# Performance work log

Hardware: AMD Instinct MI355X
Metric: run time of the kernel (lower is better)

Reference implementation:

```python
import jax, jax.numpy as jnp
import numpy as np

T, B = 50, 512
S, A, BEL, H, E, M = 256, 32, 1024, 1024, 1024, 256
MIN_STD = 0.1


def setup_inputs() -> dict:
    key = jax.random.key(0)
    ks = jax.random.split(key, 24)
    def rn(k, shape, scale=1.0):
        return jax.random.normal(k, shape, dtype=jnp.float32) * scale
    w = 0.05  # weight init scale
    return {
        "prev_state": rn(ks[0], (B, S)),
        "actions": rn(ks[1], (T, B, A)),
        "prev_belief": rn(ks[2], (B, BEL)),
        "observations": rn(ks[3], (T, B, E)),
        "nonterminals": jnp.ones((T, B, 1), dtype=jnp.float32),
        "map_embeddings": rn(ks[4], (T, B, M)),
        "map_embeddings_post": rn(ks[5], (T, B, M)),
        "noise_prior": rn(ks[6], (T, B, S)),
        "noise_post": rn(ks[7], (T, B, S)),
        "W_sa": rn(ks[8], (BEL, S + A + M), w), "b_sa": jnp.zeros((BEL,), jnp.float32),
        "W_ih": rn(ks[9], (3 * BEL, BEL), w), "b_ih": jnp.zeros((3 * BEL,), jnp.float32),
        "W_hh": rn(ks[10], (3 * BEL, BEL), w), "b_hh": jnp.zeros((3 * BEL,), jnp.float32),
        "W_bp": rn(ks[11], (H, BEL), w), "b_bp": jnp.zeros((H,), jnp.float32),
        "W_sp": rn(ks[12], (2 * S, H), w), "b_sp": jnp.zeros((2 * S,), jnp.float32),
        "W_bq": rn(ks[13], (H, BEL + E + M), w), "b_bq": jnp.zeros((H,), jnp.float32),
        "W_sq": rn(ks[14], (2 * S, H), w), "b_sq": jnp.zeros((2 * S,), jnp.float32),
    }


def reference(prev_state, actions, prev_belief, observations, nonterminals,
              map_embeddings, map_embeddings_post, noise_prior, noise_post,
              W_sa, b_sa, W_ih, b_ih, W_hh, b_hh,
              W_bp, b_bp, W_sp, b_sp, W_bq, b_bq, W_sq, b_sq):
    relu = jax.nn.relu
    def lin(x, W, b):
        return x @ W.T + b

    def gru(x, h):  # torch.nn.GRUCell math
        gi = x @ W_ih.T + b_ih
        gh = h @ W_hh.T + b_hh
        i_r, i_z, i_n = jnp.split(gi, 3, axis=1)
        h_r, h_z, h_n = jnp.split(gh, 3, axis=1)
        r = jax.nn.sigmoid(i_r + h_r)
        z = jax.nn.sigmoid(i_z + h_z)
        n = jnp.tanh(i_n + r * h_n)
        return (1.0 - z) * n + z * h

    def std(raw):
        return jnp.minimum(jax.nn.softplus(raw) + MIN_STD, 5.0)

    def step(carry, xs):
        belief, post_state = carry
        a, obs, nt, me, mp, np_, nq = xs
        s = post_state * nt
        hid = relu(lin(jnp.concatenate([s, a, me], axis=1), W_sa, b_sa))
        belief = gru(hid, belief)
        # prior p(z_t | h_t)
        hp = relu(lin(belief, W_bp, b_bp))
        p_mean, p_raw = jnp.split(lin(hp, W_sp, b_sp), 2, axis=1)
        p_std = std(p_raw)
        p_state = p_mean + p_std * np_
        # posterior q(z_t | h_t, e_t, m_t)
        hq = relu(lin(jnp.concatenate([belief, obs, mp], axis=1), W_bq, b_bq))
        q_mean, q_raw = jnp.split(lin(hq, W_sq, b_sq), 2, axis=1)
        q_std = std(q_raw)
        q_state = q_mean + q_std * nq
        return (belief, q_state), (belief, p_state, p_mean, p_std, q_state, q_mean, q_std)

    _, outs = jax.lax.scan(
        step, (prev_belief, prev_state),
        (actions, observations, nonterminals, map_embeddings,
         map_embeddings_post, noise_prior, noise_post))
    return outs  # 7 arrays, each (T, B, *)
```

## Files before the change

### kernel.cpp

```cpp
#include <hip/hip_runtime.h>
#include <hip/hip_bf16.h>

#define NT 50
#define NB 512
#define SD 256
#define BD 1024
#define HD 1024
#define ED 1024
#define MD 256
#define NBLK 512
#define PGSZ (1024 * 256)
#define K1BIG 0x40000000

typedef __attribute__((ext_vector_type(8))) short bf16x8;
typedef __attribute__((ext_vector_type(4))) float f32x4;

__device__ __forceinline__ void gload_lds16(const void* g, void* l) {
  __builtin_amdgcn_global_load_lds(
      (const __attribute__((address_space(1))) void*)g,
      (__attribute__((address_space(3))) void*)l, 16, 0, 0);
}
__device__ __forceinline__ void gload_lds16_sc0(const void* g, void* l) {
  __builtin_amdgcn_global_load_lds(
      (const __attribute__((address_space(1))) void*)g,
      (__attribute__((address_space(3))) void*)l, 16, 0, 1);
}

__device__ __forceinline__ void aload16(const void* a, f32x4* r) {
  asm volatile("global_load_dwordx4 %0, %1, off sc0" : "=&v"(*r) : "v"(a) : "memory");
}
__device__ __forceinline__ void aload4(const void* a, float* r) {
  asm volatile("global_load_dword %0, %1, off sc0" : "=&v"(*r) : "v"(a) : "memory");
}
#define VMWAIT(N)                                        \
  asm volatile("s_waitcnt vmcnt(" #N ")" ::: "memory");  \
  __builtin_amdgcn_sched_barrier(0);

__device__ __forceinline__ void astore16(void* g, f32x4 v) {
  asm volatile("global_store_dwordx4 %0, %1, off sc0" :: "v"(g), "v"(v) : "memory");
}
__device__ __forceinline__ void astore4(void* g, float v) {
  asm volatile("global_store_dword %0, %1, off sc0" :: "v"(g), "v"(v) : "memory");
}
__device__ __forceinline__ void astore2(void* g, unsigned v) {
  asm volatile("global_store_short %0, %1, off sc0" :: "v"(g), "v"(v) : "memory");
}
__device__ __forceinline__ void ntstore16(void* g, f32x4 v) {
  asm volatile("global_store_dwordx4 %0, %1, off nt" :: "v"(g), "v"(v) : "memory");
}
__device__ __forceinline__ void ntstore4(void* g, float v) {
  asm volatile("global_store_dword %0, %1, off nt" :: "v"(g), "v"(v) : "memory");
}

__device__ __forceinline__ float sigmoidf_(float x) { return 1.0f / (1.0f + __expf(-x)); }
__device__ __forceinline__ float softplusf_(float x) {
  return (x > 0.0f) ? (x + log1pf(__expf(-x))) : log1pf(__expf(x));
}
__device__ __forceinline__ unsigned short bfb(float x) {
  __hip_bfloat16 h = __float2bfloat16(x);
  return __builtin_bit_cast(unsigned short, h);
}

__device__ __forceinline__ void xbar(unsigned* cnt, int inst, int xcd, int nx) {
  asm volatile("s_waitcnt vmcnt(0) lgkmcnt(0)" ::: "memory");
  __syncthreads();
  if (threadIdx.x == 0) {
    unsigned* c = cnt + 256 + (size_t)(inst * 8 + xcd) * 16;
    __hip_atomic_fetch_add(c, 1u, __ATOMIC_RELAXED, __HIP_MEMORY_SCOPE_AGENT);
    while (__hip_atomic_load(c, __ATOMIC_RELAXED, __HIP_MEMORY_SCOPE_AGENT) < (unsigned)nx)
      __builtin_amdgcn_s_sleep(2);
  }
  __syncthreads();
}

__device__ __noinline__ void gemm64(
    int EPI, char* lds,
    const __hip_bfloat16* __restrict__ A1, int lda1,
    const __hip_bfloat16* __restrict__ A2, int lda2, int K1,
    const __hip_bfloat16* __restrict__ Wr, int ldw, int nIter,
    const float* __restrict__ bias, const float* __restrict__ Cadd,
    float* __restrict__ Cf, __hip_bfloat16* __restrict__ Cb, int ldc, int m0) {
  const int tid = threadIdx.x;
  const int lane = tid & 63, w = tid >> 6;
  const int wr = w >> 1, wc = w & 1;
  f32x4 acc[2][2] = {};
  const __hip_bfloat16* a1r = A1 + (size_t)(m0 + lane) * lda1;
  const __hip_bfloat16* a2r = A2 ? (A2 + (size_t)(m0 + lane) * lda2) : a1r;
  const __hip_bfloat16* wrow = Wr + (size_t)lane * ldw;

  auto stage = [&](int it) {
    const int k0 = it << 6;
    char* la = lds + (size_t)(it % 3) * 16384;
    char* lb = la + 8192;
    const __hip_bfloat16* as = (k0 < K1) ? (a1r + k0) : (a2r + (k0 - K1));
    gload_lds16_sc0(as + (2 * w) * 8, la + (2 * w) * 1024);
    gload_lds16_sc0(as + (2 * w + 1) * 8, la + (2 * w + 1) * 1024);
    gload_lds16(wrow + k0 + (2 * w) * 8, lb + (2 * w) * 1024);
    gload_lds16(wrow + k0 + (2 * w + 1) * 8, lb + (2 * w + 1) * 1024);
  };

  __syncthreads();
  stage(0);
  stage(1);
  VMWAIT(4)
  __builtin_amdgcn_s_barrier();
  __builtin_amdgcn_sched_barrier(0);

  const int kq = lane >> 4, r15 = lane & 15;
  for (int i = 0; i < nIter; ++i) {
    if (i + 2 < nIter) stage(i + 2);
    const char* la = lds + (size_t)(i % 3) * 16384;
    const char* lb = la + 8192;
#pragma unroll
    for (int s = 0; s < 2; ++s) {
      bf16x8 af[2], bfr[2];
#pragma unroll
      for (int m = 0; m < 2; ++m)
        af[m] = *(const bf16x8*)(la + (size_t)((s * 4 + kq) * 64 + wr * 32 + m * 16 + r15) * 16);
#pragma unroll
      for (int n = 0; n < 2; ++n)
        bfr[n] = *(const bf16x8*)(lb + (size_t)((s * 4 + kq) * 64 + wc * 32 + n * 16 + r15) * 16);
#pragma unroll
      for (int m = 0; m < 2; ++m)
#pragma unroll
        for (int n = 0; n < 2; ++n)
          acc[m][n] = __builtin_amdgcn_mfma_f32_16x16x32_bf16(af[m], bfr[n], acc[m][n], 0, 0, 0);
    }
    if (i + 1 < nIter) {
      if (i + 2 < nIter) {
        VMWAIT(4)
      } else {
        VMWAIT(0)
      }
      __builtin_amdgcn_s_barrier();
      __builtin_amdgcn_sched_barrier(0);
    }
  }

  const int rg = lane >> 4;
  float ad[2][2][4];
  if (EPI == 3) {
#pragma unroll
    for (int m = 0; m < 2; ++m)
#pragma unroll
      for (int n = 0; n < 2; ++n) {
        const int col = wc * 32 + n * 16 + r15;
#pragma unroll
        for (int i2 = 0; i2 < 4; ++i2) {
          const int row = m0 + wr * 32 + m * 16 + rg * 4 + i2;
          aload4(Cadd + (size_t)row * ldc + col, &ad[m][n][i2]);
        }
      }
    VMWAIT(0)
  }
#pragma unroll
  for (int m = 0; m < 2; ++m) {
#pragma unroll
    for (int n = 0; n < 2; ++n) {
      const int col = wc * 32 + n * 16 + r15;
      const float bv = bias ? bias[col] : 0.0f;
#pragma unroll
      for (int i2 = 0; i2 < 4; ++i2) {
        const int row = m0 + wr * 32 + m * 16 + rg * 4 + i2;
        float v = acc[m][n][i2] + bv;
        if (EPI == 3) v += ad[m][n][i2];
        if (EPI != 0) {
          v = v > 0.0f ? v : 0.0f;
          astore2(Cb + (size_t)row * ldc + col, (unsigned)bfb(v));
        } else {
          astore4(Cf + (size_t)row * ldc + col, v);
        }
      }
    }
  }
}

__device__ __noinline__ void gemm_head64(
    char* lds, const __hip_bfloat16* __restrict__ A,
    const __hip_bfloat16* __restrict__ Wr, const float* __restrict__ bias,
    const float* __restrict__ noise, float* __restrict__ st_o, float* __restrict__ mn_o,
    float* __restrict__ sd_o, const float* __restrict__ ntn,
    __hip_bfloat16* __restrict__ sprev, int isq, int n0, int m0) {
  const int tid = threadIdx.x;
  const int lane = tid & 63, w = tid >> 6;
  const int wr = w >> 1, wc = w & 1;
  f32x4 acc[2][2] = {};
  const __hip_bfloat16* ar = A + (size_t)(m0 + lane) * BD;
  const __hip_bfloat16* wrow = Wr + (size_t)lane * BD;

  auto stage = [&](int it) {
    const int k0 = it << 6;
    char* la = lds + (size_t)(it % 3) * 16384;
    char* lb = la + 8192;
    gload_lds16_sc0(ar + k0 + (2 * w) * 8, la + (2 * w) * 1024);
    gload_lds16_sc0(ar + k0 + (2 * w + 1) * 8, la + (2 * w + 1) * 1024);
    gload_lds16(wrow + k0 + (2 * w) * 8, lb + (2 * w) * 1024);
    gload_lds16(wrow + k0 + (2 * w + 1) * 8, lb + (2 * w + 1) * 1024);
  };

  __syncthreads();
  stage(0);
  stage(1);
  VMWAIT(4)
  __builtin_amdgcn_s_barrier();
  __builtin_amdgcn_sched_barrier(0);

  const int kq = lane >> 4, r15 = lane & 15;
  for (int i = 0; i < 16; ++i) {
    if (i + 2 < 16) stage(i + 2);
    const char* la = lds + (size_t)(i % 3) * 16384;
    const char* lb = la + 8192;
#pragma unroll
    for (int s = 0; s < 2; ++s) {
      bf16x8 af[2], bfr[2];
#pragma unroll
      for (int m = 0; m < 2; ++m)
        af[m] = *(const bf16x8*)(la + (size_t)((s * 4 + kq) * 64 + wr * 32 + m * 16 + r15) * 16);
#pragma unroll
      for (int n = 0; n < 2; ++n)
        bfr[n] = *(const bf16x8*)(lb + (size_t)((s * 4 + kq) * 64 + wc * 32 + n * 16 + r15) * 16);
#pragma unroll
      for (int m = 0; m < 2; ++m)
#pragma unroll
        for (int n = 0; n < 2; ++n)
          acc[m][n] = __builtin_amdgcn_mfma_f32_16x16x32_bf16(af[m], bfr[n], acc[m][n], 0, 0, 0);
    }
    if (i + 1 < 16) {
      if (i + 2 < 16) {
        VMWAIT(4)
      } else {
        VMWAIT(0)
      }
      __builtin_amdgcn_s_barrier();
      __builtin_amdgcn_sched_barrier(0);
    }
  }

  const int rg = lane >> 4;
  const bool even = (r15 & 1) == 0;
#pragma unroll
  for (int m = 0; m < 2; ++m) {
#pragma unroll
    for (int n = 0; n < 2; ++n) {
      const int col = n0 + wc * 32 + n * 16 + r15;
      const int j = col >> 1;
      const float bv = bias[col];
#pragma unroll
      for (int i2 = 0; i2 < 4; ++i2) {
        const int row = m0 + wr * 32 + m * 16 + rg * 4 + i2;
        float v = acc[m][n][i2] + bv;
        float partner = __shfl_xor(v, 1);
        float mean = even ? v : partner;
        float raw = even ? partner : v;
        float sd = fminf(softplusf_(raw) + 0.1f, 5.0f);
        const size_t o = (size_t)row * SD + j;
        if (even) {
          float st = mean + sd * noise[o];
          ntstore4(mn_o + o, mean);
          ntstore4(st_o + o, st);
          if (isq) astore2(sprev + o, (unsigned)bfb(st * ntn[row]));
        } else {
          ntstore4(sd_o + o, sd);
        }
      }
    }
  }
}

struct Args {
  const float *prev_state, *actions, *prev_belief, *observations, *nonterminals,
      *me, *mp, *noise_p, *noise_q,
      *W_sa, *b_sa, *W_ih, *b_ih, *W_hh, *b_hh,
      *W_bp, *b_bp, *W_sp, *b_sp, *W_bq, *b_bq, *W_sq, *b_sq;
  float* out;
  unsigned* cnt;
  __hip_bfloat16 *Wsa, *Wih, *Whh, *Wbp, *Wbq, *Wsp, *Wsq;
  __hip_bfloat16 *actme, *obsmp, *sprev, *bel, *hid, *hpb, *hqb;
  float *gi, *gh, *hq_obs;
  float *bsp_ro, *bsq_ro;
};

__global__ __launch_bounds__(256) void prep(Args P) {
  const int gtid = blockIdx.x * 256 + threadIdx.x;
  for (int i = gtid; i < BD * 576; i += PGSZ) {
    int r = i / 576, k = i - r * 576;
    P.Wsa[i] = __float2bfloat16(k < 544 ? P.W_sa[(size_t)r * 544 + k] : 0.0f);
  }
  for (int i = gtid; i < 3 * BD * BD; i += PGSZ) P.Wih[i] = __float2bfloat16(P.W_ih[i]);
  for (int i = gtid; i < 3 * BD * BD; i += PGSZ) P.Whh[i] = __float2bfloat16(P.W_hh[i]);
  for (int i = gtid; i < HD * BD; i += PGSZ) P.Wbp[i] = __float2bfloat16(P.W_bp[i]);
  for (int i = gtid; i < HD * 2304; i += PGSZ) P.Wbq[i] = __float2bfloat16(P.W_bq[i]);
  for (int i = gtid; i < 512 * HD; i += PGSZ) {
    int r = i >> 10, k = i & 1023;
    int dr = (r < 256) ? (2 * r) : (2 * (r - 256) + 1);
    P.Wsp[(size_t)dr * 1024 + k] = __float2bfloat16(P.W_sp[i]);
    P.Wsq[(size_t)dr * 1024 + k] = __float2bfloat16(P.W_sq[i]);
  }
  for (int i = gtid; i < 512; i += PGSZ) {
    int dr = (i < 256) ? (2 * i) : (2 * (i - 256) + 1);
    P.bsp_ro[dr] = P.b_sp[i];
    P.bsq_ro[dr] = P.b_sq[i];
  }
  for (int i = gtid; i < NT * NB * 320; i += PGSZ) {
    int tb = i / 320, j = i - tb * 320;
    float v = (j < 32) ? P.actions[(size_t)tb * 32 + j]
                       : (j < 288 ? P.me[(size_t)tb * 256 + (j - 32)] : 0.0f);
    P.actme[i] = __float2bfloat16(v);
  }
  for (int i = gtid; i < NB * 1280; i += PGSZ) {
    int bb = i / 1280, j = i - bb * 1280;
    float v = (j < ED) ? P.observations[(size_t)bb * ED + j] : P.mp[(size_t)bb * MD + (j - ED)];
    P.obsmp[i] = __float2bfloat16(v);
  }
  for (int i = gtid; i < NB * SD; i += PGSZ) {
    int r = i >> 8;
    P.sprev[i] = __float2bfloat16(P.prev_state[i] * P.nonterminals[r]);
  }
  for (int i = gtid; i < NB * BD; i += PGSZ) P.bel[i] = __float2bfloat16(P.prev_belief[i]);
}

__global__ __launch_bounds__(256, 2) void mega(Args P) {
  __shared__ alignas(16) char lds[49152];
  __shared__ int sh[3];
  const int tid = threadIdx.x;

  if (tid == 0) {
    unsigned x;
    asm volatile("s_getreg_b32 %0, hwreg(HW_REG_XCC_ID)" : "=s"(x));
    x &= 7u;
    unsigned s = __hip_atomic_fetch_add(P.cnt + x * 16, 1u, __ATOMIC_RELAXED,
                                        __HIP_MEMORY_SCOPE_AGENT);
    sh[0] = (int)x;
    sh[1] = (int)s;
  }
  __syncthreads();
  const int xcd = sh[0], slot = sh[1];

  if (tid == 0) {
    __hip_atomic_fetch_add(P.cnt + 128, 1u, __ATOMIC_RELAXED, __HIP_MEMORY_SCOPE_AGENT);
    while (__hip_atomic_load(P.cnt + 128, __ATOMIC_RELAXED, __HIP_MEMORY_SCOPE_AGENT) <
           (unsigned)NBLK)
      __builtin_amdgcn_s_sleep(4);
    sh[2] = (int)__hip_atomic_load(P.cnt + xcd * 16, __ATOMIC_RELAXED,
                                   __HIP_MEMORY_SCOPE_AGENT);
  }
  __syncthreads();
  const int nx = sh[2];
  const int m0 = xcd * 64;
  const size_t o_ps = (size_t)NT * NB * BD;
  const size_t blk = (size_t)NT * NB * SD;

  for (int t = 0; t < NT; ++t) {
    const int inst = t * 5;
    for (int tt = slot; tt < 64; tt += nx) {
      if (tt < 16) {
        const int n = tt;
        gemm64(1, lds, P.sprev, SD, P.actme + (size_t)t * NB * 320, 320, 256,
               P.Wsa + (size_t)n * 64 * 576, 576, 9,
               P.b_sa + n * 64, nullptr, nullptr, P.hid + n * 64, BD, m0);
      } else {
        const int n = tt - 16;
        gemm64(0, lds, P.bel, BD, nullptr, 0, K1BIG,
               P.Whh + (size_t)n * 64 * BD, BD, 16,
               P.b_hh + n * 64, nullptr, P.gh + n * 64, nullptr, 3 * BD, m0);
      }
    }
    xbar(P.cnt, inst + 0, xcd, nx);
    for (int tt = slot; tt < 64; tt += nx) {
      if (tt < 48) {
        const int n = tt;
        gemm64(0, lds, P.hid, BD, nullptr, 0, K1BIG,
               P.Wih + (size_t)n * 64 * BD, BD, 16,
               P.b_ih + n * 64, nullptr, P.gi + n * 64, nullptr, 3 * BD, m0);
      } else {
        const int n = tt - 48;
        gemm64(0, lds, P.obsmp, 1280, nullptr, 0, K1BIG,
               P.Wbq + (size_t)n * 64 * 2304 + 1024, 2304, 20,
               nullptr, nullptr, P.hq_obs + n * 64, nullptr, 1024, m0);
      }
    }
    xbar(P.cnt, inst + 1, xcd, nx);
    for (int u = slot * 256 + tid; u < 8192; u += nx * 256) {
      const int r = m0 + (u >> 7), j0 = (u & 127) << 3;
      const float* gib = P.gi + (size_t)r * 3072 + j0;
      const float* ghb = P.gh + (size_t)r * 3072 + j0;
      f32x4 ir0, ir1, iz0, iz1, in0, in1, hr0, hr1, hz0, hz1, hn0, hn1, hbv;
      aload16(gib, &ir0);
      aload16(gib + 4, &ir1);
      aload16(gib + 1024, &iz0);
      aload16(gib + 1028, &iz1);
      aload16(gib + 2048, &in0);
      aload16(gib + 2052, &in1);
      aload16(ghb, &hr0);
      aload16(ghb + 4, &hr1);
      aload16(ghb + 1024, &hz0);
      aload16(ghb + 1028, &hz1);
      aload16(ghb + 2048, &hn0);
      aload16(ghb + 2052, &hn1);
      aload16(P.bel + (size_t)r * BD + j0, &hbv);
      VMWAIT(0)
      bf16x8 hb = __builtin_bit_cast(bf16x8, hbv);
      float o[8];
      unsigned short nb[8];
#pragma unroll
      for (int k = 0; k < 8; ++k) {
        float gr = (k < 4 ? ir0[k] : ir1[k - 4]) + (k < 4 ? hr0[k] : hr1[k - 4]);
        float gz = (k < 4 ? iz0[k] : iz1[k - 4]) + (k < 4 ? hz0[k] : hz1[k - 4]);
        float hn = (k < 4 ? hn0[k] : hn1[k - 4]);
        float in_ = (k < 4 ? in0[k] : in1[k - 4]);
        float r_ = sigmoidf_(gr);
        float z_ = sigmoidf_(gz);
        float n_ = tanhf(in_ + r_ * hn);
        __hip_bfloat16 hv16 = __builtin_bit_cast(__hip_bfloat16, (unsigned short)hb[k]);
        float hv = __bfloat162float(hv16);
        float bel = (1.0f - z_) * n_ + z_ * hv;
        o[k] = bel;
        nb[k] = bfb(bel);
      }
      float* ob = P.out + (size_t)t * NB * BD + (size_t)r * BD + j0;
      ntstore16(ob, f32x4{o[0], o[1], o[2], o[3]});
      ntstore16(ob + 4, f32x4{o[4], o[5], o[6], o[7]});
      astore16(P.bel + (size_t)r * BD + j0, __builtin_bit_cast(f32x4, *(bf16x8*)nb));
    }
    if (t + 1 < NT) {
      for (int v = slot * 256 + tid; v < 5120; v += nx * 256) {
        const int r = m0 + v / 80, c0 = (v % 80) << 4;
        const float* src = (c0 < ED)
            ? (P.observations + (size_t)(t + 1) * NB * ED + (size_t)r * ED + c0)
            : (P.mp + (size_t)(t + 1) * NB * MD + (size_t)r * MD + (c0 - ED));
        unsigned short nb[16];
#pragma unroll
        for (int q = 0; q < 4; ++q) {
          f32x4 vv = *(const f32x4*)(src + q * 4);
#pragma unroll
          for (int kk = 0; kk < 4; ++kk) nb[q * 4 + kk] = bfb(vv[kk]);
        }
        astore16(P.obsmp + (size_t)r * 1280 + c0, __builtin_bit_cast(f32x4, *(bf16x8*)nb));
        astore16(P.obsmp + (size_t)r * 1280 + c0 + 8,
                 __builtin_bit_cast(f32x4, *(bf16x8*)(nb + 8)));
      }
    }
    xbar(P.cnt, inst + 2, xcd, nx);
    for (int tt = slot; tt < 32; tt += nx) {
      if (tt < 16) {
        const int n = tt;
        gemm64(1, lds, P.bel, BD, nullptr, 0, K1BIG,
               P.Wbp + (size_t)n * 64 * BD, BD, 16,
               P.b_bp + n * 64, nullptr, nullptr, P.hpb + n * 64, HD, m0);
      } else {
        const int n = tt - 16;
        gemm64(3, lds, P.bel, BD, nullptr, 0, K1BIG,
               P.Wbq + (size_t)n * 64 * 2304, 2304, 16,
               P.b_bq + n * 64, P.hq_obs + n * 64, nullptr, P.hqb + n * 64, HD, m0);
      }
    }
    xbar(P.cnt, inst + 3, xcd, nx);
    {
      const float* ntn = P.nonterminals + (size_t)((t + 1 < NT) ? t + 1 : t) * NB;
      const size_t to = (size_t)t * NB * SD;
      for (int tt = slot; tt < 16; tt += nx) {
        if (tt < 8)
          gemm_head64(lds, P.hpb, P.Wsp + (size_t)tt * 64 * BD, P.bsp_ro,
                      P.noise_p + to, P.out + o_ps + to, P.out + o_ps + blk + to,
                      P.out + o_ps + 2 * blk + to, ntn, P.sprev, 0, tt * 64, m0);
        else
          gemm_head64(lds, P.hqb, P.Wsq + (size_t)(tt - 8) * 64 * BD, P.bsq_ro,
                      P.noise_q + to, P.out + o_ps + 3 * blk + to,
                      P.out + o_ps + 4 * blk + to, P.out + o_ps + 5 * blk + to,
                      ntn, P.sprev, 1, (tt - 8) * 64, m0);
      }
    }
    xbar(P.cnt, inst + 4, xcd, nx);
  }
}


extern "C" void kernel_launch(void* const* d_in, const int* in_sizes, int n_in,
                              void* d_out, int out_size, void* d_ws, size_t ws_size,
                              hipStream_t stream) {
  Args P;
  P.prev_state = (const float*)d_in[0];
  P.actions = (const float*)d_in[1];
  P.prev_belief = (const float*)d_in[2];
  P.observations = (const float*)d_in[3];
  P.nonterminals = (const float*)d_in[4];
  P.me = (const float*)d_in[5];
  P.mp = (const float*)d_in[6];
  P.noise_p = (const float*)d_in[7];
  P.noise_q = (const float*)d_in[8];
  P.W_sa = (const float*)d_in[9];  P.b_sa = (const float*)d_in[10];
  P.W_ih = (const float*)d_in[11]; P.b_ih = (const float*)d_in[12];
  P.W_hh = (const float*)d_in[13]; P.b_hh = (const float*)d_in[14];
  P.W_bp = (const float*)d_in[15]; P.b_bp = (const float*)d_in[16];
  P.W_sp = (const float*)d_in[17]; P.b_sp = (const float*)d_in[18];
  P.W_bq = (const float*)d_in[19]; P.b_bq = (const float*)d_in[20];
  P.W_sq = (const float*)d_in[21]; P.b_sq = (const float*)d_in[22];
  P.out = (float*)d_out;

  char* p = (char*)d_ws;
  auto carve = [&](size_t bytes) -> char* {
    char* r = p;
    p += (bytes + 255) & ~(size_t)255;
    return r;
  };
  const size_t cnt_bytes = (size_t)65536 * 4;
  P.cnt = (unsigned*)carve(cnt_bytes);
  P.Wsa = (__hip_bfloat16*)carve((size_t)BD * 576 * 2);
  P.Wih = (__hip_bfloat16*)carve((size_t)3 * BD * BD * 2);
  P.Whh = (__hip_bfloat16*)carve((size_t)3 * BD * BD * 2);
  P.Wbp = (__hip_bfloat16*)carve((size_t)HD * BD * 2);
  P.Wbq = (__hip_bfloat16*)carve((size_t)HD * 2304 * 2);
  P.Wsp = (__hip_bfloat16*)carve((size_t)512 * HD * 2);
  P.Wsq = (__hip_bfloat16*)carve((size_t)512 * HD * 2);
  P.bsp_ro = (float*)carve(512 * 4);
  P.bsq_ro = (float*)carve(512 * 4);
  P.actme = (__hip_bfloat16*)carve((size_t)NT * NB * 320 * 2);
  P.obsmp = (__hip_bfloat16*)carve((size_t)NB * 1280 * 2);
  P.sprev = (__hip_bfloat16*)carve((size_t)NB * SD * 2);
  P.bel = (__hip_bfloat16*)carve((size_t)NB * BD * 2);
  P.hid = (__hip_bfloat16*)carve((size_t)NB * BD * 2);
  P.hpb = (__hip_bfloat16*)carve((size_t)NB * HD * 2);
  P.hqb = (__hip_bfloat16*)carve((size_t)NB * HD * 2);
  P.gi = (float*)carve((size_t)NB * 3 * BD * 4);
  P.gh = (float*)carve((size_t)NB * 3 * BD * 4);
  P.hq_obs = (float*)carve((size_t)NB * HD * 4);

  hipMemsetAsync(P.cnt, 0, cnt_bytes, stream);
  prep<<<1024, 256, 0, stream>>>(P);
  mega<<<NBLK, 256, 0, stream>>>(P);
}
```

Before: 5.311 ms.

## Use dynamic atomic job queues per XCD and raise persistent grid to 768 blocks

Replaces the static round-robin tile assignment in each GEMM phase with a per-XCD atomic ticket counter, so blocks grab 64-row tiles dynamically. Raises the persistent grid from 512 to 768 blocks, with launch bounds allowing 3 blocks per CU, and lengthens spin-wait sleeps. The aim is better load balance and more concurrent workers per barrier phase. In exchange it adds two __syncthreads and an atomic per job, needs fresh counter regions in the workspace, and risks register pressure from the tighter occupancy target.

```diff
diff --git a/kernel.cpp b/kernel.cpp
--- a/kernel.cpp
+++ b/kernel.cpp
@@ -8,7 +8,7 @@
 #define HD 1024
 #define ED 1024
 #define MD 256
-#define NBLK 512
+#define NBLK 768
 #define PGSZ (1024 * 256)
 #define K1BIG 0x40000000
 
@@ -68,7 +68,7 @@
     unsigned* c = cnt + 256 + (size_t)(inst * 8 + xcd) * 16;
     __hip_atomic_fetch_add(c, 1u, __ATOMIC_RELAXED, __HIP_MEMORY_SCOPE_AGENT);
     while (__hip_atomic_load(c, __ATOMIC_RELAXED, __HIP_MEMORY_SCOPE_AGENT) < (unsigned)nx)
-      __builtin_amdgcn_s_sleep(2);
+      __builtin_amdgcn_s_sleep(16);
   }
   __syncthreads();
 }
@@ -164,11 +164,11 @@
         const int row = m0 + wr * 32 + m * 16 + rg * 4 + i2;
         float v = acc[m][n][i2] + bv;
         if (EPI == 3) v += ad[m][n][i2];
-        if (EPI != 0) {
+        if (EPI == 0) {
+          astore4(Cf + (size_t)row * ldc + col, v);
+        } else {
           v = v > 0.0f ? v : 0.0f;
           astore2(Cb + (size_t)row * ldc + col, (unsigned)bfb(v));
-        } else {
-          astore4(Cf + (size_t)row * ldc + col, v);
         }
       }
     }
@@ -319,9 +319,9 @@
   for (int i = gtid; i < NB * BD; i += PGSZ) P.bel[i] = __float2bfloat16(P.prev_belief[i]);
 }
 
-__global__ __launch_bounds__(256, 2) void mega(Args P) {
+__global__ __launch_bounds__(256, 3) void mega(Args P) {
   __shared__ alignas(16) char lds[49152];
-  __shared__ int sh[3];
+  __shared__ int sh[4];
   const int tid = threadIdx.x;
 
   if (tid == 0) {
@@ -340,7 +340,7 @@
     __hip_atomic_fetch_add(P.cnt + 128, 1u, __ATOMIC_RELAXED, __HIP_MEMORY_SCOPE_AGENT);
     while (__hip_atomic_load(P.cnt + 128, __ATOMIC_RELAXED, __HIP_MEMORY_SCOPE_AGENT) <
            (unsigned)NBLK)
-      __builtin_amdgcn_s_sleep(4);
+      __builtin_amdgcn_s_sleep(16);
     sh[2] = (int)__hip_atomic_load(P.cnt + xcd * 16, __ATOMIC_RELAXED,
                                    __HIP_MEMORY_SCOPE_AGENT);
   }
@@ -350,33 +350,54 @@
   const size_t o_ps = (size_t)NT * NB * BD;
   const size_t blk = (size_t)NT * NB * SD;
 
+#define NEXTJOB(tk, J, out_j)                                                              \
+  {                                                                                        \
+    __syncthreads();                                                                       \
+    if (tid == 0)                                                                          \
+      sh[3] = (int)__hip_atomic_fetch_add((tk), 1u, __ATOMIC_RELAXED,                      \
+                                          __HIP_MEMORY_SCOPE_AGENT);                       \
+    __syncthreads();                                                                       \
+    out_j = (sh[3] < (J)) ? sh[3] : -1;                                                    \
+  }
+
   for (int t = 0; t < NT; ++t) {
     const int inst = t * 5;
-    for (int tt = slot; tt < 64; tt += nx) {
-      if (tt < 16) {
-        const int n = tt;
-        gemm64(1, lds, P.sprev, SD, P.actme + (size_t)t * NB * 320, 320, 256,
-               P.Wsa + (size_t)n * 64 * 576, 576, 9,
-               P.b_sa + n * 64, nullptr, nullptr, P.hid + n * 64, BD, m0);
-      } else {
-        const int n = tt - 16;
-        gemm64(0, lds, P.bel, BD, nullptr, 0, K1BIG,
-               P.Whh + (size_t)n * 64 * BD, BD, 16,
-               P.b_hh + n * 64, nullptr, P.gh + n * 64, nullptr, 3 * BD, m0);
+    unsigned* tkbase = P.cnt + 32768;
+    {
+      unsigned* tk = tkbase + (size_t)((t * 5 + 0) * 8 + xcd) * 16;
+      for (;;) {
+        int j;
+        NEXTJOB(tk, 64, j)
+        if (j < 0) break;
+        if (j < 16) {
+          gemm64(1, lds, P.sprev, SD, P.actme + (size_t)t * NB * 320, 320, 256,
+                 P.Wsa + (size_t)j * 64 * 576, 576, 9,
+                 P.b_sa + j * 64, nullptr, nullptr, P.hid + j * 64, BD, m0);
+        } else {
+          const int n = j - 16;
+          gemm64(0, lds, P.bel, BD, nullptr, 0, K1BIG,
+                 P.Whh + (size_t)n * 64 * BD, BD, 16,
+                 P.b_hh + n * 64, nullptr, P.gh + n * 64, nullptr, 3 * BD, m0);
+        }
       }
     }
     xbar(P.cnt, inst + 0, xcd, nx);
-    for (int tt = slot; tt < 64; tt += nx) {
-      if (tt < 48) {
-        const int n = tt;
-        gemm64(0, lds, P.hid, BD, nullptr, 0, K1BIG,
-               P.Wih + (size_t)n * 64 * BD, BD, 16,
-               P.b_ih + n * 64, nullptr, P.gi + n * 64, nullptr, 3 * BD, m0);
-      } else {
-        const int n = tt - 48;
-        gemm64(0, lds, P.obsmp, 1280, nullptr, 0, K1BIG,
-               P.Wbq + (size_t)n * 64 * 2304 + 1024, 2304, 20,
-               nullptr, nullptr, P.hq_obs + n * 64, nullptr, 1024, m0);
+    {
+      unsigned* tk = tkbase + (size_t)((t * 5 + 1) * 8 + xcd) * 16;
+      for (;;) {
+        int j;
+        NEXTJOB(tk, 64, j)
+        if (j < 0) break;
+        if (j < 48) {
+          gemm64(0, lds, P.hid, BD, nullptr, 0, K1BIG,
+                 P.Wih + (size_t)j * 64 * BD, BD, 16,
+                 P.b_ih + j * 64, nullptr, P.gi + j * 64, nullptr, 3 * BD, m0);
+        } else {
+          const int n = j - 48;
+          gemm64(0, lds, P.obsmp, 1280, nullptr, 0, K1BIG,
+                 P.Wbq + (size_t)n * 64 * 2304 + 1024, 2304, 20,
+                 nullptr, nullptr, P.hq_obs + n * 64, nullptr, 1024, m0);
+        }
       }
     }
     xbar(P.cnt, inst + 1, xcd, nx);
@@ -441,33 +462,42 @@
       }
     }
     xbar(P.cnt, inst + 2, xcd, nx);
-    for (int tt = slot; tt < 32; tt += nx) {
-      if (tt < 16) {
-        const int n = tt;
-        gemm64(1, lds, P.bel, BD, nullptr, 0, K1BIG,
-               P.Wbp + (size_t)n * 64 * BD, BD, 16,
-               P.b_bp + n * 64, nullptr, nullptr, P.hpb + n * 64, HD, m0);
-      } else {
-        const int n = tt - 16;
-        gemm64(3, lds, P.bel, BD, nullptr, 0, K1BIG,
-               P.Wbq + (size_t)n * 64 * 2304, 2304, 16,
-               P.b_bq + n * 64, P.hq_obs + n * 64, nullptr, P.hqb + n * 64, HD, m0);
+    {
+      unsigned* tk = tkbase + (size_t)((t * 5 + 3) * 8 + xcd) * 16;
+      for (;;) {
+        int j;
+        NEXTJOB(tk, 32, j)
+        if (j < 0) break;
+        if (j < 16) {
+          gemm64(1, lds, P.bel, BD, nullptr, 0, K1BIG,
+                 P.Wbp + (size_t)j * 64 * BD, BD, 16,
+                 P.b_bp + j * 64, nullptr, nullptr, P.hpb + j * 64, HD, m0);
+        } else {
+          const int n = j - 16;
+          gemm64(3, lds, P.bel, BD, nullptr, 0, K1BIG,
+                 P.Wbq + (size_t)n * 64 * 2304, 2304, 16,
+                 P.b_bq + n * 64, P.hq_obs + n * 64, nullptr, P.hqb + n * 64, HD, m0);
+        }
       }
     }
     xbar(P.cnt, inst + 3, xcd, nx);
     {
       const float* ntn = P.nonterminals + (size_t)((t + 1 < NT) ? t + 1 : t) * NB;
       const size_t to = (size_t)t * NB * SD;
-      for (int tt = slot; tt < 16; tt += nx) {
-        if (tt < 8)
-          gemm_head64(lds, P.hpb, P.Wsp + (size_t)tt * 64 * BD, P.bsp_ro,
+      unsigned* tk = tkbase + (size_t)((t * 5 + 4) * 8 + xcd) * 16;
+      for (;;) {
+        int j;
+        NEXTJOB(tk, 16, j)
+        if (j < 0) break;
+        if (j < 8)
+          gemm_head64(lds, P.hpb, P.Wsp + (size_t)j * 64 * BD, P.bsp_ro,
                       P.noise_p + to, P.out + o_ps + to, P.out + o_ps + blk + to,
-                      P.out + o_ps + 2 * blk + to, ntn, P.sprev, 0, tt * 64, m0);
+                      P.out + o_ps + 2 * blk + to, ntn, P.sprev, 0, j * 64, m0);
         else
-          gemm_head64(lds, P.hqb, P.Wsq + (size_t)(tt - 8) * 64 * BD, P.bsq_ro,
+          gemm_head64(lds, P.hqb, P.Wsq + (size_t)(j - 8) * 64 * BD, P.bsq_ro,
                       P.noise_q + to, P.out + o_ps + 3 * blk + to,
                       P.out + o_ps + 4 * blk + to, P.out + o_ps + 5 * blk + to,
-                      ntn, P.sprev, 1, (tt - 8) * 64, m0);
+                      ntn, P.sprev, 1, (j - 8) * 64, m0);
       }
     }
     xbar(P.cnt, inst + 4, xcd, nx);
```

Measured after the change: 7.341 ms. 1.38x slower.

## Prefetch first weight k-tiles into dedicated LDS during grid barrier waits

Applied to the files above, without the earlier changes.

Adds a separate LDS region that holds the first three 64-wide k-chunks of the next phase's weight tile. Each block issues these loads while it spins at the cross-block barrier, so the next GEMM can begin without waiting on weight latency. The GEMM pipeline is reorganised to issue three A stages up front and read the first B stages from the prefetch buffer. LDS grows from 48KB to 72KB, which may reduce occupancy at two blocks per CU, and the vmcnt bookkeeping becomes more delicate.

```diff
diff --git a/kernel.cpp b/kernel.cpp
--- a/kernel.cpp
+++ b/kernel.cpp
@@ -11,6 +11,7 @@
 #define NBLK 512
 #define PGSZ (1024 * 256)
 #define K1BIG 0x40000000
+#define WPRE_OFF 49152
 
 typedef __attribute__((ext_vector_type(8))) short bf16x8;
 typedef __attribute__((ext_vector_type(4))) float f32x4;
@@ -61,12 +62,28 @@
   return __builtin_bit_cast(unsigned short, h);
 }
 
-__device__ __forceinline__ void xbar(unsigned* cnt, int inst, int xcd, int nx) {
+__device__ __forceinline__ void wpre_issue(const __hip_bfloat16* W, int ldw,
+                                           char* lds, int tid) {
+  const int w = tid >> 6, lane = tid & 63;
+  const __hip_bfloat16* wrow = W + (size_t)lane * ldw;
+  char* wpre = lds + WPRE_OFF;
+#pragma unroll
+  for (int c = 0; c < 3; ++c) {
+    gload_lds16(wrow + (c << 6) + (2 * w) * 8, wpre + c * 8192 + (2 * w) * 1024);
+    gload_lds16(wrow + (c << 6) + (2 * w + 1) * 8, wpre + c * 8192 + (2 * w + 1) * 1024);
+  }
+}
+
+__device__ __forceinline__ void xbar_pf(unsigned* cnt, int inst, int xcd, int nx,
+                                        const __hip_bfloat16* nextW, int nextLdw,
+                                        char* lds, int tid) {
   asm volatile("s_waitcnt vmcnt(0) lgkmcnt(0)" ::: "memory");
   __syncthreads();
-  if (threadIdx.x == 0) {
-    unsigned* c = cnt + 256 + (size_t)(inst * 8 + xcd) * 16;
+  unsigned* c = cnt + 256 + (size_t)(inst * 8 + xcd) * 16;
+  if (tid == 0)
     __hip_atomic_fetch_add(c, 1u, __ATOMIC_RELAXED, __HIP_MEMORY_SCOPE_AGENT);
+  if (nextW) wpre_issue(nextW, nextLdw, lds, tid);
+  if (tid == 0) {
     while (__hip_atomic_load(c, __ATOMIC_RELAXED, __HIP_MEMORY_SCOPE_AGENT) < (unsigned)nx)
       __builtin_amdgcn_s_sleep(2);
   }
@@ -74,7 +91,7 @@
 }
 
 __device__ __noinline__ void gemm64(
-    int EPI, char* lds,
+    int EPI, char* lds, bool pre,
     const __hip_bfloat16* __restrict__ A1, int lda1,
     const __hip_bfloat16* __restrict__ A2, int lda2, int K1,
     const __hip_bfloat16* __restrict__ Wr, int ldw, int nIter,
@@ -87,8 +104,16 @@
   const __hip_bfloat16* a1r = A1 + (size_t)(m0 + lane) * lda1;
   const __hip_bfloat16* a2r = A2 ? (A2 + (size_t)(m0 + lane) * lda2) : a1r;
   const __hip_bfloat16* wrow = Wr + (size_t)lane * ldw;
-
-  auto stage = [&](int it) {
+  char* wpre = lds + WPRE_OFF;
+
+  auto aissue = [&](int it) {
+    const int k0 = it << 6;
+    char* la = lds + (size_t)(it % 3) * 16384;
+    const __hip_bfloat16* as = (k0 < K1) ? (a1r + k0) : (a2r + (k0 - K1));
+    gload_lds16_sc0(as + (2 * w) * 8, la + (2 * w) * 1024);
+    gload_lds16_sc0(as + (2 * w + 1) * 8, la + (2 * w + 1) * 1024);
+  };
+  auto stageAW = [&](int it) {
     const int k0 = it << 6;
     char* la = lds + (size_t)(it % 3) * 16384;
     char* lb = la + 8192;
@@ -100,17 +125,18 @@
   };
 
   __syncthreads();
-  stage(0);
-  stage(1);
+  if (!pre) wpre_issue(Wr, ldw, lds, tid);
+  aissue(0);
+  aissue(1);
+  aissue(2);
   VMWAIT(4)
   __builtin_amdgcn_s_barrier();
   __builtin_amdgcn_sched_barrier(0);
 
   const int kq = lane >> 4, r15 = lane & 15;
   for (int i = 0; i < nIter; ++i) {
-    if (i + 2 < nIter) stage(i + 2);
     const char* la = lds + (size_t)(i % 3) * 16384;
-    const char* lb = la + 8192;
+    const char* lb = (i < 3) ? (wpre + (size_t)i * 8192) : (la + 8192);
 #pragma unroll
     for (int s = 0; s < 2; ++s) {
       bf16x8 af[2], bfr[2];
@@ -127,13 +153,16 @@
           acc[m][n] = __builtin_amdgcn_mfma_f32_16x16x32_bf16(af[m], bfr[n], acc[m][n], 0, 0, 0);
     }
     if (i + 1 < nIter) {
-      if (i + 2 < nIter) {
+      if (i == 0) {
+        VMWAIT(2)
+      } else if (i + 2 < nIter) {
         VMWAIT(4)
       } else {
         VMWAIT(0)
       }
       __builtin_amdgcn_s_barrier();
       __builtin_amdgcn_sched_barrier(0);
+      if (i + 3 < nIter) stageAW(i + 3);
     }
   }
 
@@ -164,11 +193,11 @@
         const int row = m0 + wr * 32 + m * 16 + rg * 4 + i2;
         float v = acc[m][n][i2] + bv;
         if (EPI == 3) v += ad[m][n][i2];
-        if (EPI != 0) {
+        if (EPI == 0) {
+          astore4(Cf + (size_t)row * ldc + col, v);
+        } else {
           v = v > 0.0f ? v : 0.0f;
           astore2(Cb + (size_t)row * ldc + col, (unsigned)bfb(v));
-        } else {
-          astore4(Cf + (size_t)row * ldc + col, v);
         }
       }
     }
@@ -176,7 +205,7 @@
 }
 
 __device__ __noinline__ void gemm_head64(
-    char* lds, const __hip_bfloat16* __restrict__ A,
+    char* lds, bool pre, const __hip_bfloat16* __restrict__ A,
     const __hip_bfloat16* __restrict__ Wr, const float* __restrict__ bias,
     const float* __restrict__ noise, float* __restrict__ st_o, float* __restrict__ mn_o,
     float* __restrict__ sd_o, const float* __restrict__ ntn,
@@ -187,8 +216,15 @@
   f32x4 acc[2][2] = {};
   const __hip_bfloat16* ar = A + (size_t)(m0 + lane) * BD;
   const __hip_bfloat16* wrow = Wr + (size_t)lane * BD;
-
-  auto stage = [&](int it) {
+  char* wpre = lds + WPRE_OFF;
+
+  auto aissue = [&](int it) {
+    const int k0 = it << 6;
+    char* la = lds + (size_t)(it % 3) * 16384;
+    gload_lds16_sc0(ar + k0 + (2 * w) * 8, la + (2 * w) * 1024);
+    gload_lds16_sc0(ar + k0 + (2 * w + 1) * 8, la + (2 * w + 1) * 1024);
+  };
+  auto stageAW = [&](int it) {
     const int k0 = it << 6;
     char* la = lds + (size_t)(it % 3) * 16384;
     char* lb = la + 8192;
@@ -199,17 +235,18 @@
   };
 
   __syncthreads();
-  stage(0);
-  stage(1);
+  if (!pre) wpre_issue(Wr, BD, lds, tid);
+  aissue(0);
+  aissue(1);
+  aissue(2);
   VMWAIT(4)
   __builtin_amdgcn_s_barrier();
   __builtin_amdgcn_sched_barrier(0);
 
   const int kq = lane >> 4, r15 = lane & 15;
   for (int i = 0; i < 16; ++i) {
-    if (i + 2 < 16) stage(i + 2);
     const char* la = lds + (size_t)(i % 3) * 16384;
-    const char* lb = la + 8192;
+    const char* lb = (i < 3) ? (wpre + (size_t)i * 8192) : (la + 8192);
 #pragma unroll
     for (int s = 0; s < 2; ++s) {
       bf16x8 af[2], bfr[2];
@@ -226,13 +263,16 @@
           acc[m][n] = __builtin_amdgcn_mfma_f32_16x16x32_bf16(af[m], bfr[n], acc[m][n], 0, 0, 0);
     }
     if (i + 1 < 16) {
-      if (i + 2 < 16) {
+      if (i == 0) {
+        VMWAIT(2)
+      } else if (i + 2 < 16) {
         VMWAIT(4)
       } else {
         VMWAIT(0)
       }
       __builtin_amdgcn_s_barrier();
       __builtin_amdgcn_sched_barrier(0);
+      if (i + 3 < 16) stageAW(i + 3);
     }
   }
 
@@ -320,8 +360,8 @@
 }
 
 __global__ __launch_bounds__(256, 2) void mega(Args P) {
-  __shared__ alignas(16) char lds[49152];
-  __shared__ int sh[3];
+  __shared__ alignas(16) char lds[73728];
+  __shared__ int sh[4];
   const int tid = threadIdx.x;
 
   if (tid == 0) {
@@ -350,36 +390,51 @@
   const size_t o_ps = (size_t)NT * NB * BD;
   const size_t blk = (size_t)NT * NB * SD;
 
+  const __hip_bfloat16* wA = nullptr; int lA = 0;
+  if (slot < 16) { wA = P.Wsa + (size_t)slot * 64 * 576; lA = 576; }
+  else if (slot < 64) { wA = P.Whh + (size_t)(slot - 16) * 64 * BD; lA = BD; }
+  const __hip_bfloat16* wB = nullptr; int lB = 0;
+  if (slot < 48) { wB = P.Wih + (size_t)slot * 64 * BD; lB = BD; }
+  else if (slot < 64) { wB = P.Wbq + (size_t)(slot - 48) * 64 * 2304 + 1024; lB = 2304; }
+  const __hip_bfloat16* wD = nullptr; int lD = 0;
+  if (slot < 16) { wD = P.Wbp + (size_t)slot * 64 * BD; lD = BD; }
+  else if (slot < 32) { wD = P.Wbq + (size_t)(slot - 16) * 64 * 2304; lD = 2304; }
+  const __hip_bfloat16* wE = nullptr; int lE = 0;
+  if (slot < 8) { wE = P.Wsp + (size_t)slot * 64 * BD; lE = BD; }
+  else if (slot < 16) { wE = P.Wsq + (size_t)(slot - 8) * 64 * BD; lE = BD; }
+
+  if (wA) wpre_issue(wA, lA, lds, tid);
+
   for (int t = 0; t < NT; ++t) {
     const int inst = t * 5;
     for (int tt = slot; tt < 64; tt += nx) {
+      const bool pre = (tt == slot);
       if (tt < 16) {
-        const int n = tt;
-        gemm64(1, lds, P.sprev, SD, P.actme + (size_t)t * NB * 320, 320, 256,
-               P.Wsa + (size_t)n * 64 * 576, 576, 9,
-               P.b_sa + n * 64, nullptr, nullptr, P.hid + n * 64, BD, m0);
+        gemm64(1, lds, pre, P.sprev, SD, P.actme + (size_t)t * NB * 320, 320, 256,
+               P.Wsa + (size_t)tt * 64 * 576, 576, 9,
+               P.b_sa + tt * 64, nullptr, nullptr, P.hid + tt * 64, BD, m0);
       } else {
         const int n = tt - 16;
-        gemm64(0, lds, P.bel, BD, nullptr, 0, K1BIG,
+        gemm64(0, lds, pre, P.bel, BD, nullptr, 0, K1BIG,
                P.Whh + (size_t)n * 64 * BD, BD, 16,
                P.b_hh + n * 64, nullptr, P.gh + n * 64, nullptr, 3 * BD, m0);
       }
     }
-    xbar(P.cnt, inst + 0, xcd, nx);
+    xbar_pf(P.cnt, inst + 0, xcd, nx, wB, lB, lds, tid);
     for (int tt = slot; tt < 64; tt += nx) {
+      const bool pre = (tt == slot);
       if (tt < 48) {
-        const int n = tt;
-        gemm64(0, lds, P.hid, BD, nullptr, 0, K1BIG,
-               P.Wih + (size_t)n * 64 * BD, BD, 16,
-               P.b_ih + n * 64, nullptr, P.gi + n * 64, nullptr, 3 * BD, m0);
+        gemm64(0, lds, pre, P.hid, BD, nullptr, 0, K1BIG,
+               P.Wih + (size_t)tt * 64 * BD, BD, 16,
+               P.b_ih + tt * 64, nullptr, P.gi + tt * 64, nullptr, 3 * BD, m0);
       } else {
         const int n = tt - 48;
-        gemm64(0, lds, P.obsmp, 1280, nullptr, 0, K1BIG,
+        gemm64(0, lds, pre, P.obsmp, 1280, nullptr, 0, K1BIG,
                P.Wbq + (size_t)n * 64 * 2304 + 1024, 2304, 20,
                nullptr, nullptr, P.hq_obs + n * 64, nullptr, 1024, m0);
       }
     }
-    xbar(P.cnt, inst + 1, xcd, nx);
+    xbar_pf(P.cnt, inst + 1, xcd, nx, wD, lD, lds, tid);
     for (int u = slot * 256 + tid; u < 8192; u += nx * 256) {
       const int r = m0 + (u >> 7), j0 = (u & 127) << 3;
       const float* gib = P.gi + (size_t)r * 3072 + j0;
@@ -440,37 +495,38 @@
                  __builtin_bit_cast(f32x4, *(bf16x8*)(nb + 8)));
       }
     }
-    xbar(P.cnt, inst + 2, xcd, nx);
+    xbar_pf(P.cnt, inst + 2, xcd, nx, nullptr, 0, lds, tid);
     for (int tt = slot; tt < 32; tt += nx) {
+      const bool pre = (tt == slot);
       if (tt < 16) {
-        const int n = tt;
-        gemm64(1, lds, P.bel, BD, nullptr, 0, K1BIG,
-               P.Wbp + (size_t)n * 64 * BD, BD, 16,
-               P.b_bp + n * 64, nullptr, nullptr, P.hpb + n * 64, HD, m0);
+        gemm64(1, lds, pre, P.bel, BD, nullptr, 0, K1BIG,
+               P.Wbp + (size_t)tt * 64 * BD, BD, 16,
+               P.b_bp + tt * 64, nullptr, nullptr, P.hpb + tt * 64, HD, m0);
       } else {
         const int n = tt - 16;
-        gemm64(3, lds, P.bel, BD, nullptr, 0, K1BIG,
+        gemm64(3, lds, pre, P.bel, BD, nullptr, 0, K1BIG,
                P.Wbq + (size_t)n * 64 * 2304, 2304, 16,
                P.b_bq + n * 64, P.hq_obs + n * 64, nullptr, P.hqb + n * 64, HD, m0);
       }
     }
-    xbar(P.cnt, inst + 3, xcd, nx);
+    xbar_pf(P.cnt, inst + 3, xcd, nx, wE, lE, lds, tid);
     {
       const float* ntn = P.nonterminals + (size_t)((t + 1 < NT) ? t + 1 : t) * NB;
       const size_t to = (size_t)t * NB * SD;
       for (int tt = slot; tt < 16; tt += nx) {
+        const bool pre = (tt == slot);
         if (tt < 8)
-          gemm_head64(lds, P.hpb, P.Wsp + (size_t)tt * 64 * BD, P.bsp_ro,
+          gemm_head64(lds, pre, P.hpb, P.Wsp + (size_t)tt * 64 * BD, P.bsp_ro,
                       P.noise_p + to, P.out + o_ps + to, P.out + o_ps + blk + to,
                       P.out + o_ps + 2 * blk + to, ntn, P.sprev, 0, tt * 64, m0);
         else
-          gemm_head64(lds, P.hqb, P.Wsq + (size_t)(tt - 8) * 64 * BD, P.bsq_ro,
+          gemm_head64(lds, pre, P.hqb, P.Wsq + (size_t)(tt - 8) * 64 * BD, P.bsq_ro,
                       P.noise_q + to, P.out + o_ps + 3 * blk + to,
                       P.out + o_ps + 4 * blk + to, P.out + o_ps + 5 * blk + to,
                       ntn, P.sprev, 1, (tt - 8) * 64, m0);
       }
     }
-    xbar(P.cnt, inst + 4, xcd, nx);
+    xbar_pf(P.cnt, inst + 4, xcd, nx, wA, lA, lds, tid);
   }
 }
 
```

After: 5.319 ms, median of 2. About the same (+0.2%).
